# Optimization experiments

Measured on AMD Instinct MI355X. Metric: run time of the kernel, lower is better.

## Reference

```python
import jax, jax.numpy as jnp
import numpy as np

B, N, D = 2, 8192, 1024
H = 16
HD = D // H  # 64
EPS = 1e-6


def setup_inputs() -> dict:
    key = jax.random.key(0)
    ks = jax.random.split(key, 5)
    scale = 1.0 / np.sqrt(D)
    return {
        "x": jax.random.normal(ks[0], (B, N, D), dtype=jnp.float32),
        "Wq": jax.random.normal(ks[1], (D, D), dtype=jnp.float32) * scale,
        "Wk": jax.random.normal(ks[2], (D, D), dtype=jnp.float32) * scale,
        "Wv": jax.random.normal(ks[3], (D, D), dtype=jnp.float32) * scale,
        "Wo": jax.random.normal(ks[4], (D, D), dtype=jnp.float32) * scale,
    }


def _feature_map(a):
    # ELU + 1 (positive feature map)
    return jax.nn.elu(a) + 1.0


def reference(x, Wq, Wk, Wv, Wo):
    b, n, d = x.shape
    # torch nn.Linear: y = x @ W.T
    q = _feature_map((x @ Wq.T).reshape(b, n, H, HD))  # (B,N,H,hd)
    k = _feature_map((x @ Wk.T).reshape(b, n, H, HD))
    v = (x @ Wv.T).reshape(b, n, H, HD)
    # global kv state per head: (B,H,hd,hd)
    kv = jnp.einsum('bnhd,bnhm->bhdm', k, v)
    k_sum = k.sum(axis=1)  # (B,H,hd)
    numerator = jnp.einsum('bnhd,bhdm->bnhm', q, kv)  # (B,N,H,hd)
    denominator = jnp.einsum('bnhd,bhd->bnh', q, k_sum)[..., None]
    out = numerator / (denominator + EPS)
    out = out.reshape(b, n, d)
    return out @ Wo.T
```

## Files before the change

### kernel.cpp

```cpp
#include <hip/hip_runtime.h>
#include <stdint.h>

#define BB 2
#define NN 8192
#define DD 1024
#define KK 1024
#define NHEAD 16
#define HDIM 64
#define KV_CHUNKS 32

using f32x4  = __attribute__((ext_vector_type(4))) float;
using bf16x8 = __attribute__((ext_vector_type(8))) short;

__device__ __forceinline__ unsigned short f2bf(float f) {
  union { float f; unsigned int u; } v; v.f = f;
  unsigned int r = v.u + 0x7fffu + ((v.u >> 16) & 1u);
  return (unsigned short)(r >> 16);
}
__device__ __forceinline__ float bf2f(unsigned short u) {
  union { unsigned int u; float f; } v; v.u = ((unsigned int)u) << 16;
  return v.f;
}

__device__ __forceinline__ void gload_lds16(const unsigned short* g, unsigned short* l) {
  __builtin_amdgcn_global_load_lds(
      (__attribute__((address_space(1))) void*)(const_cast<unsigned short*>(g)),
      (__attribute__((address_space(3))) void*)(l), 16, 0, 0);
}

__global__ __launch_bounds__(256) void convert_all(const float* __restrict__ x,
                                                   const float* __restrict__ Wq,
                                                   const float* __restrict__ Wk,
                                                   const float* __restrict__ Wv,
                                                   const float* __restrict__ Wo,
                                                   unsigned short* __restrict__ xb,
                                                   unsigned short* __restrict__ wqkv,
                                                   unsigned short* __restrict__ wob) {
  size_t i = ((size_t)blockIdx.x * 256 + threadIdx.x) * 8;
  const size_t xN = (size_t)BB * NN * DD;
  const float* src;
  unsigned short* dst;
  size_t off;
  if (i < xN) {
    src = x; dst = xb; off = i;
  } else {
    size_t r = i - xN;
    int wsel = (int)(r >> 20);
    off = r & 1048575;
    src = (wsel == 0) ? Wq : (wsel == 1) ? Wk : (wsel == 2) ? Wv : Wo;
    dst = (wsel < 3) ? (wqkv + (size_t)wsel * 1048576) : wob;
  }
  float4 a = *(const float4*)(src + off);
  float4 b = *(const float4*)(src + off + 4);
  uint32_t p0 = (uint32_t)f2bf(a.x) | ((uint32_t)f2bf(a.y) << 16);
  uint32_t p1 = (uint32_t)f2bf(a.z) | ((uint32_t)f2bf(a.w) << 16);
  uint32_t p2 = (uint32_t)f2bf(b.x) | ((uint32_t)f2bf(b.y) << 16);
  uint32_t p3 = (uint32_t)f2bf(b.z) | ((uint32_t)f2bf(b.w) << 16);
  *(uint4*)(dst + off) = make_uint4(p0, p1, p2, p3);
}

#define BAR  __builtin_amdgcn_s_barrier()
#define SB   __builtin_amdgcn_sched_barrier(0)
#define WLG  asm volatile("s_waitcnt lgkmcnt(0)" ::: "memory")
#define WVM4 asm volatile("s_waitcnt vmcnt(4)" ::: "memory")
#define WVM0 asm volatile("s_waitcnt vmcnt(0)" ::: "memory")

template <int EPI>
__global__ __launch_bounds__(512, 2) void gemm256(const unsigned short* __restrict__ A,
                                                  const unsigned short* __restrict__ Bw,
                                                  unsigned short* __restrict__ O0,
                                                  unsigned short* __restrict__ O1,
                                                  unsigned short* __restrict__ O2,
                                                  float* __restrict__ OF) {
  __shared__ unsigned short lds[2][2][2][128 * 64];
  const int t = threadIdx.x;
  const int lane = t & 63;
  const int w = t >> 6;
  const int wm = w >> 2;
  const int wn = w & 3;
  const int frow = lane & 15;
  const int g = lane >> 4;
  const int fx = frow & 7;
  const int rowBase = blockIdx.x * 256;
  const int colBase = blockIdx.y * 256;

  const int srow0 = t >> 3;
  const int ssw = ((t & 7) ^ (srow0 & 7)) * 8;
  const unsigned short* sA0 = A + (size_t)(rowBase + srow0) * KK + ssw;
  const unsigned short* sA1 = A + (size_t)(rowBase + 64 + srow0) * KK + ssw;
  const unsigned short* sB0 = Bw + (size_t)(colBase + srow0) * KK + ssw;
  const unsigned short* sB1 = Bw + (size_t)(colBase + 64 + srow0) * KK + ssw;

#define STAGE(db, ab, half, kt)                                                        \
  do {                                                                                 \
    gload_lds16(((ab) ? sB0 : sA0) + (size_t)(half) * 128 * KK + (size_t)(kt) * 64,    \
                &lds[db][ab][half][(0 * 512 + w * 64) * 8]);                           \
    gload_lds16(((ab) ? sB1 : sA1) + (size_t)(half) * 128 * KK + (size_t)(kt) * 64,    \
                &lds[db][ab][half][(1 * 512 + w * 64) * 8]);                           \
  } while (0)

  bf16x8 ar[4][2], br[4][2];
  f32x4 acc[8][4];
#pragma unroll
  for (int i = 0; i < 8; ++i)
#pragma unroll
    for (int j = 0; j < 4; ++j) acc[i][j] = (f32x4){0.f, 0.f, 0.f, 0.f};

#define LDA4(db, mih)                                                                  \
  _Pragma("unroll") for (int mi2 = 0; mi2 < 4; ++mi2)                                  \
  _Pragma("unroll") for (int kk2 = 0; kk2 < 2; ++kk2)                                  \
    ar[mi2][kk2] = *(const bf16x8*)((const char*)&lds[db][0][wm][0] +                  \
        ((mih) * 64 + mi2 * 16 + frow) * 128 + ((kk2 * 4 + g) ^ fx) * 16);

#define LDB2(db, nih)                                                                  \
  _Pragma("unroll") for (int ni2 = 0; ni2 < 2; ++ni2)                                  \
  _Pragma("unroll") for (int kk2 = 0; kk2 < 2; ++kk2)                                  \
    br[(nih) * 2 + ni2][kk2] = *(const bf16x8*)((const char*)&lds[db][1][wn >> 1][0] + \
        ((wn & 1) * 64 + (nih) * 32 + ni2 * 16 + frow) * 128 + ((kk2 * 4 + g) ^ fx) * 16);

#define MFMAQ(mih, nih)                                                                \
  __builtin_amdgcn_s_setprio(1);                                                      \
  _Pragma("unroll") for (int mi2 = 0; mi2 < 4; ++mi2)                                  \
  _Pragma("unroll") for (int ni2 = 0; ni2 < 2; ++ni2)                                  \
  _Pragma("unroll") for (int kk2 = 0; kk2 < 2; ++kk2)                                  \
    acc[(mih) * 4 + mi2][(nih) * 2 + ni2] = __builtin_amdgcn_mfma_f32_16x16x32_bf16(   \
        ar[mi2][kk2], br[(nih) * 2 + ni2][kk2],                                        \
        acc[(mih) * 4 + mi2][(nih) * 2 + ni2], 0, 0, 0);                               \
  __builtin_amdgcn_s_setprio(0);

  STAGE(0, 1, 0, 0); STAGE(0, 1, 1, 0);
  STAGE(0, 0, 0, 0); STAGE(0, 0, 1, 0);
  STAGE(1, 1, 0, 1); STAGE(1, 1, 1, 1);
  WVM4; BAR; SB;

#pragma unroll 1
  for (int i = 0; i < 8; ++i) {
    const bool full = (i < 7);
    const int kt1 = 2 * i + 1, kt2 = 2 * i + 2, kt3 = 2 * i + 3;
    LDA4(0, 0); LDB2(0, 0);
    STAGE(1, 0, 0, kt1);
    BAR; WLG; SB; MFMAQ(0, 0); BAR; SB;
    LDB2(0, 1);
    STAGE(1, 0, 1, kt1);
    BAR; WLG; SB; MFMAQ(0, 1); BAR; SB;
    LDA4(0, 1);
    if (full) STAGE(0, 1, 0, kt2);
    BAR; WLG; SB; MFMAQ(1, 0); BAR; SB;
    if (full) STAGE(0, 1, 1, kt2);
    BAR; SB; MFMAQ(1, 1);
    if (full) { WVM4; } else { WVM0; }
    BAR; SB;
    LDA4(1, 0); LDB2(1, 0);
    if (full) STAGE(0, 0, 0, kt2);
    BAR; WLG; SB; MFMAQ(0, 0); BAR; SB;
    LDB2(1, 1);
    if (full) STAGE(0, 0, 1, kt2);
    BAR; WLG; SB; MFMAQ(0, 1); BAR; SB;
    LDA4(1, 1);
    if (full) STAGE(1, 1, 0, kt3);
    BAR; WLG; SB; MFMAQ(1, 0); BAR; SB;
    if (full) STAGE(1, 1, 1, kt3);
    BAR; SB; MFMAQ(1, 1);
    if (full) { WVM4; }
    BAR; SB;
  }

  const int r0 = rowBase + wm * 128 + g * 4;
  if constexpr (EPI == 0) {
    const int ymat = blockIdx.y >> 2;
    unsigned short* dst = (ymat == 0) ? O0 : ((ymat == 1) ? O1 : O2);
    const int c0 = (blockIdx.y & 3) * 256 + wn * 64 + frow;
    const bool doElu = (ymat < 2);
#pragma unroll
    for (int mi = 0; mi < 8; ++mi)
#pragma unroll
      for (int j = 0; j < 4; ++j) {
        const size_t ro = (size_t)(r0 + mi * 16 + j) * DD;
#pragma unroll
        for (int ni = 0; ni < 4; ++ni) {
          float v = acc[mi][ni][j];
          if (doElu) v = (v > 0.f) ? (v + 1.f) : __expf(v);
          dst[ro + c0 + ni * 16] = f2bf(v);
        }
      }
  } else {
    const int c0 = colBase + wn * 64 + frow;
#pragma unroll
    for (int mi = 0; mi < 8; ++mi)
#pragma unroll
      for (int j = 0; j < 4; ++j) {
        const size_t ro = (size_t)(r0 + mi * 16 + j) * DD;
#pragma unroll
        for (int ni = 0; ni < 4; ++ni)
          OF[ro + c0 + ni * 16] = acc[mi][ni][j];
      }
  }
#undef STAGE
#undef LDA4
#undef LDB2
#undef MFMAQ
}

__global__ __launch_bounds__(256) void kv_mfma(const unsigned short* __restrict__ Kb,
                                               const unsigned short* __restrict__ Vb,
                                               float* __restrict__ kvp,
                                               float* __restrict__ ksp) {
  __shared__ unsigned short kt[2][32 * 64];
  __shared__ unsigned short vt[2][32 * 64];
  const int blk = blockIdx.x;
  const int c = blk % KV_CHUNKS;
  const int h = (blk / KV_CHUNKS) % NHEAD;
  const int b = blk / (KV_CHUNKS * NHEAD);
  const int t = threadIdx.x;
  const int lane = t & 63;
  const int w = t >> 6;
  const int frow = lane & 15;
  const int g = lane >> 4;
  const int chunkLen = NN / KV_CHUNKS;
  const int NSTEP = chunkLen / 32;

  const size_t base = ((size_t)b * NN + (size_t)c * chunkLen) * DD + h * HDIM;
  const unsigned short* sK = Kb + base + (size_t)(t >> 3) * DD + (t & 7) * 8;
  const unsigned short* sV = Vb + base + (size_t)(t >> 3) * DD + (t & 7) * 8;

  bf16x8 ones;
#pragma unroll
  for (int j = 0; j < 8; ++j) ones[j] = (short)0x3F80;

  f32x4 acc[4], aks;
#pragma unroll
  for (int mt = 0; mt < 4; ++mt) acc[mt] = (f32x4){0.f, 0.f, 0.f, 0.f};
  aks = (f32x4){0.f, 0.f, 0.f, 0.f};

  gload_lds16(sK, &kt[0][t * 8]);
  gload_lds16(sV, &vt[0][t * 8]);

#pragma unroll 1
  for (int s = 0; s < NSTEP; ++s) {
    const int cur = s & 1;
    BAR;
    if (s + 1 < NSTEP) {
      gload_lds16(sK + (size_t)(s + 1) * 32 * DD, &kt[cur ^ 1][t * 8]);
      gload_lds16(sV + (size_t)(s + 1) * 32 * DD, &vt[cur ^ 1][t * 8]);
      asm volatile("s_waitcnt vmcnt(2)" ::: "memory");
    } else {
      WVM0;
    }
    BAR; SB;

    bf16x8 a;
#pragma unroll
    for (int j = 0; j < 8; ++j)
      a[j] = (short)kt[cur][(g * 8 + j) * 64 + w * 16 + frow];
#pragma unroll
    for (int mt = 0; mt < 4; ++mt) {
      bf16x8 bfr;
#pragma unroll
      for (int j = 0; j < 8; ++j)
        bfr[j] = (short)vt[cur][(g * 8 + j) * 64 + mt * 16 + frow];
      acc[mt] = __builtin_amdgcn_mfma_f32_16x16x32_bf16(a, bfr, acc[mt], 0, 0, 0);
    }
    aks = __builtin_amdgcn_mfma_f32_16x16x32_bf16(a, ones, aks, 0, 0, 0);
  }

  float* dst = kvp + (size_t)blk * 4096;
#pragma unroll
  for (int mt = 0; mt < 4; ++mt)
#pragma unroll
    for (int j = 0; j < 4; ++j)
      dst[(w * 16 + g * 4 + j) * 64 + mt * 16 + frow] = acc[mt][j];
  if (frow == 0) {
#pragma unroll
    for (int j = 0; j < 4; ++j)
      ksp[(size_t)blk * 64 + w * 16 + g * 4 + j] = aks[j];
  }
}

__global__ __launch_bounds__(256) void kv_final(const float* __restrict__ kvp,
                                                const float* __restrict__ ksp,
                                                unsigned short* __restrict__ kvb) {
  const int bh = blockIdx.x;
  const int t = threadIdx.x;
  __shared__ float kvs[4096];
#pragma unroll
  for (int e0 = 0; e0 < 4096; e0 += 256) {
    float s = 0.f;
    for (int cI = 0; cI < KV_CHUNKS; ++cI)
      s += kvp[((size_t)bh * KV_CHUNKS + cI) * 4096 + e0 + t];
    kvs[e0 + t] = s;
  }
  __syncthreads();
  unsigned short* dst = kvb + (size_t)bh * (96 * 64);
#pragma unroll
  for (int e0 = 0; e0 < 4096; e0 += 256) {
    int e = e0 + t;
    dst[e] = f2bf(kvs[(e & 63) * 64 + (e >> 6)]);
  }
  if (t < 64) {
    float s = 0.f;
    for (int cI = 0; cI < KV_CHUNKS; ++cI)
      s += ksp[((size_t)bh * KV_CHUNKS + cI) * 64 + t];
    dst[64 * 64 + t] = f2bf(s);
  }
  for (int e0 = 65 * 64; e0 < 96 * 64; e0 += 256) {
    int e = e0 + t;
    if (e < 96 * 64) dst[e] = 0;
  }
}

__global__ __launch_bounds__(256) void attn_mfma(const unsigned short* __restrict__ Qb,
                                                 const unsigned short* __restrict__ kvb,
                                                 unsigned short* __restrict__ Ob) {
  __shared__ unsigned short Bs[96 * 64];
  __shared__ unsigned short Qs[128 * 64];
  const int t = threadIdx.x;
  const int lane = t & 63;
  const int w = t >> 6;
  const int bh = blockIdx.y;
  const int b = bh >> 4;
  const int h = bh & 15;
  const int rowBase = blockIdx.x * 128;

  const unsigned short* bsrc = kvb + (size_t)bh * (96 * 64);
#pragma unroll
  for (int r = 0; r < 3; ++r) {
    int ci = r * 256 + t;
    int row = ci >> 3, ch = ci & 7;
    gload_lds16(bsrc + row * 64 + (ch ^ (row & 7)) * 8, Bs + ci * 8);
  }
  const int sr = t >> 3, ch0 = t & 7;
#pragma unroll
  for (int i = 0; i < 4; ++i) {
    int row = i * 32 + sr;
    const unsigned short* src =
        Qb + ((size_t)(b * NN + rowBase + row)) * DD + h * HDIM + (ch0 ^ (row & 7)) * 8;
    gload_lds16(src, Qs + row * 64 + ch0 * 8);
  }
  __syncthreads();

  const int frow = lane & 15;
  const int g = lane >> 4;
  bf16x8 a[2][2];
#pragma unroll
  for (int rb = 0; rb < 2; ++rb)
#pragma unroll
    for (int kk = 0; kk < 2; ++kk)
      a[rb][kk] = *(const bf16x8*)(Qs + (rb * 64 + w * 16 + frow) * 64 + ((kk * 4 + g) ^ (lane & 7)) * 8);

  f32x4 acc[2][5];
#pragma unroll
  for (int rb = 0; rb < 2; ++rb)
#pragma unroll
    for (int c = 0; c < 5; ++c) acc[rb][c] = (f32x4){0.f, 0.f, 0.f, 0.f};
#pragma unroll
  for (int c = 0; c < 5; ++c) {
#pragma unroll
    for (int kk = 0; kk < 2; ++kk) {
      bf16x8 bf = *(const bf16x8*)(Bs + (c * 16 + frow) * 64 + ((kk * 4 + g) ^ (lane & 7)) * 8);
#pragma unroll
      for (int rb = 0; rb < 2; ++rb)
        acc[rb][c] = __builtin_amdgcn_mfma_f32_16x16x32_bf16(a[rb][kk], bf, acc[rb][c], 0, 0, 0);
    }
  }

#pragma unroll
  for (int rb = 0; rb < 2; ++rb) {
    float rden[4];
#pragma unroll
    for (int j = 0; j < 4; ++j) {
      float den = __shfl(acc[rb][4][j], g * 16, 64);
      rden[j] = 1.f / (den + 1e-6f);
    }
    const size_t obase =
        ((size_t)(b * NN + rowBase + rb * 64 + w * 16 + g * 4)) * DD + h * HDIM + frow;
#pragma unroll
    for (int c = 0; c < 4; ++c)
#pragma unroll
      for (int j = 0; j < 4; ++j)
        Ob[obase + (size_t)j * DD + c * 16] = f2bf(acc[rb][c][j] * rden[j]);
  }
}

extern "C" void kernel_launch(void* const* d_in, const int* in_sizes, int n_in,
                              void* d_out, int out_size, void* d_ws, size_t ws_size,
                              hipStream_t stream) {
  const float* x  = (const float*)d_in[0];
  const float* Wq = (const float*)d_in[1];
  const float* Wk = (const float*)d_in[2];
  const float* Wv = (const float*)d_in[3];
  const float* Wo = (const float*)d_in[4];
  float* out = (float*)d_out;

  char* ws = (char*)d_ws;
  size_t off = 0;
  auto alloc = [&](size_t bytes) -> char* {
    char* p = ws + off;
    off += (bytes + 255) & ~(size_t)255;
    return p;
  };
  const size_t xN = (size_t)BB * NN * DD;
  unsigned short* xb   = (unsigned short*)alloc(xN * 2);
  unsigned short* qb   = (unsigned short*)alloc(xN * 2);
  unsigned short* kb   = (unsigned short*)alloc(xN * 2);
  unsigned short* vb   = (unsigned short*)alloc(xN * 2);
  unsigned short* wqkv = (unsigned short*)alloc((size_t)3 * DD * DD * 2);
  unsigned short* wob  = (unsigned short*)alloc((size_t)DD * DD * 2);
  float* ksp = (float*)alloc((size_t)BB * NHEAD * KV_CHUNKS * 64 * 4);
  unsigned short* kvb = (unsigned short*)alloc((size_t)BB * NHEAD * 96 * 64 * 2);
  float* kvp = (float*)xb;
  unsigned short* ob = xb;

  const int convBlocks = (int)((xN + 4 * 1048576) / 2048);
  convert_all<<<convBlocks, 256, 0, stream>>>(x, Wq, Wk, Wv, Wo, xb, wqkv, wob);

  dim3 gq(64, 12);
  gemm256<0><<<gq, 512, 0, stream>>>(xb, wqkv, qb, kb, vb, nullptr);

  kv_mfma<<<BB * NHEAD * KV_CHUNKS, 256, 0, stream>>>(kb, vb, kvp, ksp);
  kv_final<<<BB * NHEAD, 256, 0, stream>>>(kvp, ksp, kvb);

  dim3 ga(NN / 128, BB * NHEAD);
  attn_mfma<<<ga, 256, 0, stream>>>(qb, kvb, ob);

  dim3 go(64, 4);
  gemm256<1><<<go, 512, 0, stream>>>(ob, wob, nullptr, nullptr, nullptr, out);
}
```

Baseline: 207.3 us.

## Replace interleaved 8-phase GEMM pipeline with simple per-k-tile double buffering

Replaces the hand-interleaved GEMM main loop, which split each k-tile into four load/MFMA quarters with many barriers and lgkmcnt waits, with a simpler loop. Each iteration loads all A/B fragments for one 64-wide k-tile, runs all 64 MFMAs, then issues global-to-LDS staging for tile kt+2 into the freed buffer. This removes most barriers and waits but loads more fragment registers at once (8x2 A fragments) and no longer overlaps LDS reads with MFMA inside a tile. Register pressure under launch_bounds(512,2) may rise.

```diff
diff --git a/kernel.cpp b/kernel.cpp
--- a/kernel.cpp
+++ b/kernel.cpp
@@ -61,8 +61,7 @@
 
 #define BAR  __builtin_amdgcn_s_barrier()
 #define SB   __builtin_amdgcn_sched_barrier(0)
-#define WLG  asm volatile("s_waitcnt lgkmcnt(0)" ::: "memory")
-#define WVM4 asm volatile("s_waitcnt vmcnt(4)" ::: "memory")
+#define WVM8 asm volatile("s_waitcnt vmcnt(8)" ::: "memory")
 #define WVM0 asm volatile("s_waitcnt vmcnt(0)" ::: "memory")
 
 template <int EPI>
@@ -99,69 +98,52 @@
                 &lds[db][ab][half][(1 * 512 + w * 64) * 8]);                           \
   } while (0)
 
-  bf16x8 ar[4][2], br[4][2];
   f32x4 acc[8][4];
 #pragma unroll
   for (int i = 0; i < 8; ++i)
 #pragma unroll
     for (int j = 0; j < 4; ++j) acc[i][j] = (f32x4){0.f, 0.f, 0.f, 0.f};
 
-#define LDA4(db, mih)                                                                  \
-  _Pragma("unroll") for (int mi2 = 0; mi2 < 4; ++mi2)                                  \
-  _Pragma("unroll") for (int kk2 = 0; kk2 < 2; ++kk2)                                  \
-    ar[mi2][kk2] = *(const bf16x8*)((const char*)&lds[db][0][wm][0] +                  \
-        ((mih) * 64 + mi2 * 16 + frow) * 128 + ((kk2 * 4 + g) ^ fx) * 16);
-
-#define LDB2(db, nih)                                                                  \
-  _Pragma("unroll") for (int ni2 = 0; ni2 < 2; ++ni2)                                  \
-  _Pragma("unroll") for (int kk2 = 0; kk2 < 2; ++kk2)                                  \
-    br[(nih) * 2 + ni2][kk2] = *(const bf16x8*)((const char*)&lds[db][1][wn >> 1][0] + \
-        ((wn & 1) * 64 + (nih) * 32 + ni2 * 16 + frow) * 128 + ((kk2 * 4 + g) ^ fx) * 16);
-
-#define MFMAQ(mih, nih)                                                                \
-  __builtin_amdgcn_s_setprio(1);                                                      \
-  _Pragma("unroll") for (int mi2 = 0; mi2 < 4; ++mi2)                                  \
-  _Pragma("unroll") for (int ni2 = 0; ni2 < 2; ++ni2)                                  \
-  _Pragma("unroll") for (int kk2 = 0; kk2 < 2; ++kk2)                                  \
-    acc[(mih) * 4 + mi2][(nih) * 2 + ni2] = __builtin_amdgcn_mfma_f32_16x16x32_bf16(   \
-        ar[mi2][kk2], br[(nih) * 2 + ni2][kk2],                                        \
-        acc[(mih) * 4 + mi2][(nih) * 2 + ni2], 0, 0, 0);                               \
-  __builtin_amdgcn_s_setprio(0);
-
-  STAGE(0, 1, 0, 0); STAGE(0, 1, 1, 0);
-  STAGE(0, 0, 0, 0); STAGE(0, 0, 1, 0);
-  STAGE(1, 1, 0, 1); STAGE(1, 1, 1, 1);
-  WVM4; BAR; SB;
-
+  STAGE(0, 0, 0, 0); STAGE(0, 0, 1, 0); STAGE(0, 1, 0, 0); STAGE(0, 1, 1, 0);
+  STAGE(1, 0, 0, 1); STAGE(1, 0, 1, 1); STAGE(1, 1, 0, 1); STAGE(1, 1, 1, 1);
+  WVM8; BAR; SB;
+
+  constexpr int NKT = KK / 64;
 #pragma unroll 1
-  for (int i = 0; i < 8; ++i) {
-    const bool full = (i < 7);
-    const int kt1 = 2 * i + 1, kt2 = 2 * i + 2, kt3 = 2 * i + 3;
-    LDA4(0, 0); LDB2(0, 0);
-    STAGE(1, 0, 0, kt1);
-    BAR; WLG; SB; MFMAQ(0, 0); BAR; SB;
-    LDB2(0, 1);
-    STAGE(1, 0, 1, kt1);
-    BAR; WLG; SB; MFMAQ(0, 1); BAR; SB;
-    LDA4(0, 1);
-    if (full) STAGE(0, 1, 0, kt2);
-    BAR; WLG; SB; MFMAQ(1, 0); BAR; SB;
-    if (full) STAGE(0, 1, 1, kt2);
-    BAR; SB; MFMAQ(1, 1);
-    if (full) { WVM4; } else { WVM0; }
-    BAR; SB;
-    LDA4(1, 0); LDB2(1, 0);
-    if (full) STAGE(0, 0, 0, kt2);
-    BAR; WLG; SB; MFMAQ(0, 0); BAR; SB;
-    LDB2(1, 1);
-    if (full) STAGE(0, 0, 1, kt2);
-    BAR; WLG; SB; MFMAQ(0, 1); BAR; SB;
-    LDA4(1, 1);
-    if (full) STAGE(1, 1, 0, kt3);
-    BAR; WLG; SB; MFMAQ(1, 0); BAR; SB;
-    if (full) STAGE(1, 1, 1, kt3);
-    BAR; SB; MFMAQ(1, 1);
-    if (full) { WVM4; }
+  for (int kt = 0; kt < NKT; ++kt) {
+    const int db = kt & 1;
+    const char* baseA = (const char*)&lds[db][0][wm][0];
+    const char* baseB = (const char*)&lds[db][1][wn >> 1][0];
+
+    bf16x8 ar[8][2], br[4][2];
+#pragma unroll
+    for (int kk = 0; kk < 2; ++kk) {
+#pragma unroll
+      for (int mi = 0; mi < 8; ++mi)
+        ar[mi][kk] = *(const bf16x8*)(baseA + (mi * 16 + frow) * 128 + ((kk * 4 + g) ^ fx) * 16);
+#pragma unroll
+      for (int ni = 0; ni < 4; ++ni)
+        br[ni][kk] = *(const bf16x8*)(baseB + ((wn & 1) * 64 + ni * 16 + frow) * 128 + ((kk * 4 + g) ^ fx) * 16);
+    }
+
+    __builtin_amdgcn_s_setprio(1);
+#pragma unroll
+    for (int kk = 0; kk < 2; ++kk)
+#pragma unroll
+      for (int mi = 0; mi < 8; ++mi)
+#pragma unroll
+        for (int ni = 0; ni < 4; ++ni)
+          acc[mi][ni] = __builtin_amdgcn_mfma_f32_16x16x32_bf16(ar[mi][kk], br[ni][kk], acc[mi][ni], 0, 0, 0);
+    __builtin_amdgcn_s_setprio(0);
+
+    SB; BAR;
+    if (kt + 2 < NKT) {
+      STAGE(db, 0, 0, kt + 2); STAGE(db, 0, 1, kt + 2);
+      STAGE(db, 1, 0, kt + 2); STAGE(db, 1, 1, kt + 2);
+      WVM8;
+    } else if (kt + 1 < NKT) {
+      WVM0;
+    }
     BAR; SB;
   }
 
@@ -196,9 +178,6 @@
       }
   }
 #undef STAGE
-#undef LDA4
-#undef LDB2
-#undef MFMAQ
 }
 
 __global__ __launch_bounds__(256) void kv_mfma(const unsigned short* __restrict__ Kb,
```

After: 217.9 us. 5.1% more time.

## Fuse fp32-to-bf16 conversion of x into QKV GEMM A-tile loading

Applied to the files above, without the earlier changes.

Drops the separate conversion of the activation x to bf16. The QKV GEMM now loads fp32 x straight into registers, converts it to bf16 and writes it into LDS, in a register-prefetch pipeline with adjusted vmcnt waits. Only the weights are still converted up front. This removes a full write and re-read of a 32 MB bf16 copy of x. In exchange the GEMM reads twice the A bytes from global memory (recomputed across the 12 column blocks), uses more registers, and adds VALU conversion work inside the main loop.

```diff
diff --git a/kernel.cpp b/kernel.cpp
--- a/kernel.cpp
+++ b/kernel.cpp
@@ -28,28 +28,17 @@
       (__attribute__((address_space(3))) void*)(l), 16, 0, 0);
 }
 
-__global__ __launch_bounds__(256) void convert_all(const float* __restrict__ x,
-                                                   const float* __restrict__ Wq,
-                                                   const float* __restrict__ Wk,
-                                                   const float* __restrict__ Wv,
-                                                   const float* __restrict__ Wo,
-                                                   unsigned short* __restrict__ xb,
-                                                   unsigned short* __restrict__ wqkv,
-                                                   unsigned short* __restrict__ wob) {
+__global__ __launch_bounds__(256) void convert_w(const float* __restrict__ Wq,
+                                                 const float* __restrict__ Wk,
+                                                 const float* __restrict__ Wv,
+                                                 const float* __restrict__ Wo,
+                                                 unsigned short* __restrict__ wqkv,
+                                                 unsigned short* __restrict__ wob) {
   size_t i = ((size_t)blockIdx.x * 256 + threadIdx.x) * 8;
-  const size_t xN = (size_t)BB * NN * DD;
-  const float* src;
-  unsigned short* dst;
-  size_t off;
-  if (i < xN) {
-    src = x; dst = xb; off = i;
-  } else {
-    size_t r = i - xN;
-    int wsel = (int)(r >> 20);
-    off = r & 1048575;
-    src = (wsel == 0) ? Wq : (wsel == 1) ? Wk : (wsel == 2) ? Wv : Wo;
-    dst = (wsel < 3) ? (wqkv + (size_t)wsel * 1048576) : wob;
-  }
+  int wsel = (int)(i >> 20);
+  size_t off = i & 1048575;
+  const float* src = (wsel == 0) ? Wq : (wsel == 1) ? Wk : (wsel == 2) ? Wv : Wo;
+  unsigned short* dst = (wsel < 3) ? (wqkv + (size_t)wsel * 1048576) : wob;
   float4 a = *(const float4*)(src + off);
   float4 b = *(const float4*)(src + off + 4);
   uint32_t p0 = (uint32_t)f2bf(a.x) | ((uint32_t)f2bf(a.y) << 16);
@@ -62,11 +51,13 @@
 #define BAR  __builtin_amdgcn_s_barrier()
 #define SB   __builtin_amdgcn_sched_barrier(0)
 #define WLG  asm volatile("s_waitcnt lgkmcnt(0)" ::: "memory")
-#define WVM4 asm volatile("s_waitcnt vmcnt(4)" ::: "memory")
-#define WVM0 asm volatile("s_waitcnt vmcnt(0)" ::: "memory")
+#define WVM4  asm volatile("s_waitcnt vmcnt(4)" ::: "memory")
+#define WVM12 asm volatile("s_waitcnt vmcnt(12)" ::: "memory")
+#define WVM0  asm volatile("s_waitcnt vmcnt(0)" ::: "memory")
 
 template <int EPI>
-__global__ __launch_bounds__(512, 2) void gemm256(const unsigned short* __restrict__ A,
+__global__ __launch_bounds__(512, 2) void gemm256(const float* __restrict__ A32,
+                                                  const unsigned short* __restrict__ A,
                                                   const unsigned short* __restrict__ Bw,
                                                   unsigned short* __restrict__ O0,
                                                   unsigned short* __restrict__ O1,
@@ -90,6 +81,8 @@
   const unsigned short* sA1 = A + (size_t)(rowBase + 64 + srow0) * KK + ssw;
   const unsigned short* sB0 = Bw + (size_t)(colBase + srow0) * KK + ssw;
   const unsigned short* sB1 = Bw + (size_t)(colBase + 64 + srow0) * KK + ssw;
+  const float* pA0 = A32 + (size_t)(rowBase + srow0) * KK + ssw;
+  const float* pA1 = pA0 + (size_t)64 * KK;
 
 #define STAGE(db, ab, half, kt)                                                        \
   do {                                                                                 \
@@ -97,6 +90,29 @@
                 &lds[db][ab][half][(0 * 512 + w * 64) * 8]);                           \
     gload_lds16(((ab) ? sB1 : sA1) + (size_t)(half) * 128 * KK + (size_t)(kt) * 64,    \
                 &lds[db][ab][half][(1 * 512 + w * 64) * 8]);                           \
+  } while (0)
+
+#define ALOAD(R, kt, half)                                                             \
+  do {                                                                                 \
+    const float* p0_ = pA0 + (size_t)(half) * 128 * KK + (size_t)(kt) * 64;            \
+    const float* p1_ = pA1 + (size_t)(half) * 128 * KK + (size_t)(kt) * 64;            \
+    R[0] = *(const float4*)p0_; R[1] = *(const float4*)(p0_ + 4);                      \
+    R[2] = *(const float4*)p1_; R[3] = *(const float4*)(p1_ + 4);                      \
+  } while (0)
+
+#define AWRITE(db, half, R)                                                            \
+  do {                                                                                 \
+    unsigned short* d0_ = &lds[db][0][half][t * 8];                                    \
+    uint32_t q0 = (uint32_t)f2bf(R[0].x) | ((uint32_t)f2bf(R[0].y) << 16);             \
+    uint32_t q1 = (uint32_t)f2bf(R[0].z) | ((uint32_t)f2bf(R[0].w) << 16);             \
+    uint32_t q2 = (uint32_t)f2bf(R[1].x) | ((uint32_t)f2bf(R[1].y) << 16);             \
+    uint32_t q3 = (uint32_t)f2bf(R[1].z) | ((uint32_t)f2bf(R[1].w) << 16);             \
+    *(uint4*)d0_ = make_uint4(q0, q1, q2, q3);                                         \
+    uint32_t q4 = (uint32_t)f2bf(R[2].x) | ((uint32_t)f2bf(R[2].y) << 16);             \
+    uint32_t q5 = (uint32_t)f2bf(R[2].z) | ((uint32_t)f2bf(R[2].w) << 16);             \
+    uint32_t q6 = (uint32_t)f2bf(R[3].x) | ((uint32_t)f2bf(R[3].y) << 16);             \
+    uint32_t q7 = (uint32_t)f2bf(R[3].z) | ((uint32_t)f2bf(R[3].w) << 16);             \
+    *(uint4*)(d0_ + 4096) = make_uint4(q4, q5, q6, q7);                                \
   } while (0)
 
   bf16x8 ar[4][2], br[4][2];
@@ -128,40 +144,65 @@
         acc[(mih) * 4 + mi2][(nih) * 2 + ni2], 0, 0, 0);                               \
   __builtin_amdgcn_s_setprio(0);
 
-  STAGE(0, 1, 0, 0); STAGE(0, 1, 1, 0);
-  STAGE(0, 0, 0, 0); STAGE(0, 0, 1, 0);
-  STAGE(1, 1, 0, 1); STAGE(1, 1, 1, 1);
-  WVM4; BAR; SB;
+  float4 a0r[4], a1r[4], b0r[4], b1r[4];
+
+  if constexpr (EPI == 0) {
+    ALOAD(a0r, 0, 0); ALOAD(a1r, 0, 1);
+    STAGE(0, 1, 0, 0); STAGE(0, 1, 1, 0);
+    STAGE(1, 1, 0, 1); STAGE(1, 1, 1, 1);
+    ALOAD(b0r, 1, 0); ALOAD(b1r, 1, 1);
+    AWRITE(0, 0, a0r); AWRITE(0, 1, a1r);
+    WLG;
+    WVM12;
+    BAR; SB;
+  } else {
+    STAGE(0, 1, 0, 0); STAGE(0, 1, 1, 0);
+    STAGE(0, 0, 0, 0); STAGE(0, 0, 1, 0);
+    STAGE(1, 1, 0, 1); STAGE(1, 1, 1, 1);
+    WVM4; BAR; SB;
+  }
 
 #pragma unroll 1
   for (int i = 0; i < 8; ++i) {
     const bool full = (i < 7);
     const int kt1 = 2 * i + 1, kt2 = 2 * i + 2, kt3 = 2 * i + 3;
     LDA4(0, 0); LDB2(0, 0);
-    STAGE(1, 0, 0, kt1);
+    if constexpr (EPI == 0) { AWRITE(1, 0, b0r); } else { STAGE(1, 0, 0, kt1); }
     BAR; WLG; SB; MFMAQ(0, 0); BAR; SB;
     LDB2(0, 1);
-    STAGE(1, 0, 1, kt1);
+    if constexpr (EPI == 0) { AWRITE(1, 1, b1r); } else { STAGE(1, 0, 1, kt1); }
     BAR; WLG; SB; MFMAQ(0, 1); BAR; SB;
     LDA4(0, 1);
-    if (full) STAGE(0, 1, 0, kt2);
+    if (full) {
+      STAGE(0, 1, 0, kt2);
+      if constexpr (EPI == 0) ALOAD(a0r, kt2, 0);
+    }
     BAR; WLG; SB; MFMAQ(1, 0); BAR; SB;
-    if (full) STAGE(0, 1, 1, kt2);
+    if (full) {
+      STAGE(0, 1, 1, kt2);
+      if constexpr (EPI == 0) ALOAD(a1r, kt2, 1);
+    }
     BAR; SB; MFMAQ(1, 1);
-    if (full) { WVM4; } else { WVM0; }
+    if (full) { if constexpr (EPI == 0) { WVM12; } else { WVM4; } } else { WVM0; }
     BAR; SB;
     LDA4(1, 0); LDB2(1, 0);
-    if (full) STAGE(0, 0, 0, kt2);
+    if constexpr (EPI == 0) { if (full) AWRITE(0, 0, a0r); } else { if (full) STAGE(0, 0, 0, kt2); }
     BAR; WLG; SB; MFMAQ(0, 0); BAR; SB;
     LDB2(1, 1);
-    if (full) STAGE(0, 0, 1, kt2);
+    if constexpr (EPI == 0) { if (full) AWRITE(0, 1, a1r); } else { if (full) STAGE(0, 0, 1, kt2); }
     BAR; WLG; SB; MFMAQ(0, 1); BAR; SB;
     LDA4(1, 1);
-    if (full) STAGE(1, 1, 0, kt3);
+    if (full) {
+      STAGE(1, 1, 0, kt3);
+      if constexpr (EPI == 0) ALOAD(b0r, kt3, 0);
+    }
     BAR; WLG; SB; MFMAQ(1, 0); BAR; SB;
-    if (full) STAGE(1, 1, 1, kt3);
+    if (full) {
+      STAGE(1, 1, 1, kt3);
+      if constexpr (EPI == 0) ALOAD(b1r, kt3, 1);
+    }
     BAR; SB; MFMAQ(1, 1);
-    if (full) { WVM4; }
+    if (full) { if constexpr (EPI == 0) { WVM12; } else { WVM4; } }
     BAR; SB;
   }
 
@@ -196,6 +237,8 @@
       }
   }
 #undef STAGE
+#undef ALOAD
+#undef AWRITE
 #undef LDA4
 #undef LDB2
 #undef MFMAQ
@@ -399,7 +442,7 @@
     return p;
   };
   const size_t xN = (size_t)BB * NN * DD;
-  unsigned short* xb   = (unsigned short*)alloc(xN * 2);
+  unsigned short* scr  = (unsigned short*)alloc(xN * 2);
   unsigned short* qb   = (unsigned short*)alloc(xN * 2);
   unsigned short* kb   = (unsigned short*)alloc(xN * 2);
   unsigned short* vb   = (unsigned short*)alloc(xN * 2);
@@ -407,14 +450,13 @@
   unsigned short* wob  = (unsigned short*)alloc((size_t)DD * DD * 2);
   float* ksp = (float*)alloc((size_t)BB * NHEAD * KV_CHUNKS * 64 * 4);
   unsigned short* kvb = (unsigned short*)alloc((size_t)BB * NHEAD * 96 * 64 * 2);
-  float* kvp = (float*)xb;
-  unsigned short* ob = xb;
-
-  const int convBlocks = (int)((xN + 4 * 1048576) / 2048);
-  convert_all<<<convBlocks, 256, 0, stream>>>(x, Wq, Wk, Wv, Wo, xb, wqkv, wob);
+  float* kvp = (float*)scr;
+  unsigned short* ob = scr;
+
+  convert_w<<<(4 * 1024 * 1024) / 2048, 256, 0, stream>>>(Wq, Wk, Wv, Wo, wqkv, wob);
 
   dim3 gq(64, 12);
-  gemm256<0><<<gq, 512, 0, stream>>>(xb, wqkv, qb, kb, vb, nullptr);
+  gemm256<0><<<gq, 512, 0, stream>>>(x, nullptr, wqkv, qb, kb, vb, nullptr);
 
   kv_mfma<<<BB * NHEAD * KV_CHUNKS, 256, 0, stream>>>(kb, vb, kvp, ksp);
   kv_final<<<BB * NHEAD, 256, 0, stream>>>(kvp, ksp, kvb);
@@ -423,5 +465,5 @@
   attn_mfma<<<ga, 256, 0, stream>>>(qb, kvb, ob);
 
   dim3 go(64, 4);
-  gemm256<1><<<go, 512, 0, stream>>>(ob, wob, nullptr, nullptr, nullptr, out);
-}
+  gemm256<1><<<go, 512, 0, stream>>>(nullptr, ob, wob, nullptr, nullptr, nullptr, out);
+}
```

Result: slower. 554.2 us (+167.4%).
